# Optimization experiments

Measured on AMD Instinct MI355X. Metric: run time of the kernel, lower is better.

Reference implementation:

```python
import jax, jax.numpy as jnp
import numpy as np

N_GRAPHS = 262144
NPG = 6          # players per Rocket League graph
N_NODES = N_GRAPHS * NPG
HIDDEN = 32
FEAT = 4


def _build_edges():
    # fully-connected directed edges within each 6-node graph (30 per graph)
    s, d = np.meshgrid(np.arange(NPG), np.arange(NPG), indexing='ij')
    m = s != d
    ts, td = s[m], d[m]                      # [30]
    off = (np.arange(N_GRAPHS, dtype=np.int64) * NPG)[:, None]
    src = (ts[None, :] + off).reshape(-1)
    dst = (td[None, :] + off).reshape(-1)
    return np.stack([src, dst]).astype(np.int32)  # [2, E]


def setup_inputs() -> dict:
    key = jax.random.key(0)
    ks = jax.random.split(key, 10)
    edge_index = jnp.asarray(_build_edges())
    E = edge_index.shape[1]
    batch = jnp.asarray(np.repeat(np.arange(N_GRAPHS, dtype=np.int32), NPG))
    return {
        'x': jax.random.normal(ks[0], (N_NODES, FEAT), dtype=jnp.float32),
        'edge_index': edge_index,
        'edge_weight': jax.random.uniform(ks[1], (E,), dtype=jnp.float32),
        'batch': batch,
        'W1': jax.random.normal(ks[2], (FEAT, HIDDEN), dtype=jnp.float32) * 0.5,
        'b1': jax.random.normal(ks[3], (HIDDEN,), dtype=jnp.float32) * 0.1,
        'W2': jax.random.normal(ks[4], (HIDDEN, HIDDEN), dtype=jnp.float32) * 0.18,
        'b2': jax.random.normal(ks[5], (HIDDEN,), dtype=jnp.float32) * 0.1,
        'Wo': jax.random.normal(ks[6], (HIDDEN, 1), dtype=jnp.float32) * 0.18,
        'bo': jax.random.normal(ks[7], (1,), dtype=jnp.float32) * 0.1,
        'Wb': jax.random.normal(ks[8], (HIDDEN, 1), dtype=jnp.float32) * 0.18,
        'bb': jax.random.normal(ks[9], (1,), dtype=jnp.float32) * 0.1,
    }


def _gcn_conv(x, W, b, src, dst, w, n_nodes):
    # PyG GCNConv: symmetric normalization with self-loops already appended
    h = x @ W                                            # [N, out]
    deg = jax.ops.segment_sum(w, dst, num_segments=n_nodes)
    dinv = jnp.where(deg > 0, jax.lax.rsqrt(deg), 0.0)
    norm = dinv[src] * w * dinv[dst]                     # [E]
    agg = jax.ops.segment_sum(norm[:, None] * h[src], dst, num_segments=n_nodes)
    return agg + b


def reference(x, edge_index, edge_weight, batch, W1, b1, W2, b2, Wo, bo, Wb, bb):
    n = x.shape[0]
    loop = jnp.arange(n, dtype=edge_index.dtype)
    src = jnp.concatenate([edge_index[0], loop])
    dst = jnp.concatenate([edge_index[1], loop])
    w = jnp.concatenate([edge_weight, jnp.ones((n,), edge_weight.dtype)])

    h = jax.nn.relu(_gcn_conv(x, W1, b1, src, dst, w, n))
    h = jax.nn.relu(_gcn_conv(h, W2, b2, src, dst, w, n))

    # global mean pool by graph
    n_graphs = N_GRAPHS
    sums = jax.ops.segment_sum(h, batch, num_segments=n_graphs)
    cnt = jax.ops.segment_sum(jnp.ones((n,), h.dtype), batch, num_segments=n_graphs)
    pooled = sums / jnp.maximum(cnt, 1.0)[:, None]       # [G, 32]

    orange = jax.nn.sigmoid(pooled @ Wo + bo)            # [G, 1]
    blue = jax.nn.sigmoid(pooled @ Wb + bb)              # [G, 1]
    return orange, blue
```

## Files before the change

kernel.cpp:

```cpp
#include <hip/hip_runtime.h>
#include <hip/hip_bf16.h>

#define G_TOTAL 262144
#define ITERS   2
#define WAVES   4
#define NBLK    4096

typedef short s8v __attribute__((ext_vector_type(8)));
typedef float f4v __attribute__((ext_vector_type(4)));

#define MFMA16(a,b,c) __builtin_amdgcn_mfma_f32_16x16x32_bf16(a,b,c,0,0,0)

__device__ __forceinline__ unsigned short f2bf(float f){
    union { __hip_bfloat16 h; unsigned short u; } cv;
    cv.h = __float2bfloat16(f);
    return cv.u;
}
__device__ __forceinline__ unsigned int pk2(float a, float b){
    return (unsigned int)f2bf(a) | ((unsigned int)f2bf(b) << 16);
}

union FragU { s8v s; uint4 u; };

#define ARENA 9728

__global__ __launch_bounds__(256, 4)
void gcn_wave(const float* __restrict__ x,
              const float* __restrict__ ew,
              const float* __restrict__ W1,
              const float* __restrict__ b1,
              const float* __restrict__ W2,
              const float* __restrict__ b2,
              const float* __restrict__ Wo,
              const float* __restrict__ bo,
              const float* __restrict__ Wb,
              const float* __restrict__ bb,
              float* __restrict__ out)
{
    __shared__ __align__(16) unsigned char LDS[WAVES*ARENA];
    __shared__ float obuf[2][64];

    const int tid = threadIdx.x;
    const int w   = tid >> 6;
    const int l   = tid & 63;
    const int lr  = l & 15;
    const int lq  = l >> 4;

    unsigned char* AR = LDS + w*ARENA;
    unsigned short* h1RW  = (unsigned short*)AR;
    float*          rsumW = (float*)AR;
    unsigned short* actTW = (unsigned short*)(AR + 5120);

    const int gB = l >> 3, dB = l & 7;
    const bool bandOK = (dB < 6);
    const int dBc = bandOK ? dB : 0;
    int eoff0, eoff1, eoff2, eoff3, eoff4, eoff5;
    {
        int eo[6];
        #pragma unroll
        for (int s = 0; s < 6; ++s)
            eo[s] = (s == dBc) ? gB*30
                               : gB*30 + s*5 + (dBc - (dBc > s ? 1 : 0));
        eoff0=eo[0]; eoff1=eo[1]; eoff2=eo[2]; eoff3=eo[3]; eoff4=eo[4]; eoff5=eo[5];
    }
    const int bstore = (gB*6 + dBc)*40 + 32;
    const bool dnOK = (lq == 0) && ((lr & 7) < 6);
    int xoff[4];
    {
        const int dn  = lr & 7;
        const int dnc = (dn < 6) ? dn : 0;
        #pragma unroll
        for (int mt = 0; mt < 4; ++mt)
            xoff[mt] = (2*mt + (lr >> 3))*24 + dnc*4;
    }
    const bool aggB  = (lq == (lr >> 3)) && ((lr & 7) < 6);
    const int  boffL = (lq*6 + (lr & 7))*40 + 32;

    s8v w1f[2], w2f[2];
    #pragma unroll
    for (int nt = 0; nt < 2; ++nt) {
        #pragma unroll
        for (int e = 0; e < 8; ++e) {
            const int k = lq*8 + e, col = lr + 16*nt;
            w1f[nt][e] = (k < 4) ? (short)f2bf(W1[k*32 + col]) : (short)0;
            w2f[nt][e] = (short)f2bf(W2[k*32 + col]);
        }
    }
    f4v cb1[2], cb2[2];
    float wor[2][4], wbr[2][4];
    #pragma unroll
    for (int mt = 0; mt < 2; ++mt)
        #pragma unroll
        for (int j = 0; j < 4; ++j) {
            const int ch = 16*mt + lq*4 + j;
            cb1[mt][j] = b1[ch];  cb2[mt][j] = b2[ch];
            wor[mt][j] = Wo[ch];  wbr[mt][j] = Wb[ch];
        }
    const float boS = bo[0], bbS = bb[0];

    const long base = (long)blockIdx.x*(32*ITERS) + w*8;

    float evl[2][6];
    uint2 xB[2][4];

    {
        const long gb30 = base*30;
        evl[0][0] = ew[gb30 + eoff0];  evl[0][1] = ew[gb30 + eoff1];
        evl[0][2] = ew[gb30 + eoff2];  evl[0][3] = ew[gb30 + eoff3];
        evl[0][4] = ew[gb30 + eoff4];  evl[0][5] = ew[gb30 + eoff5];
        if (lq == 0) {
            const float* xp = x + base*24;
            #pragma unroll
            for (int mt = 0; mt < 4; ++mt) {
                const float4 xv = *(const float4*)(xp + xoff[mt]);
                xB[0][mt] = make_uint2(pk2(xv.x, xv.y), pk2(xv.z, xv.w));
            }
        }
    }

    #pragma unroll
    for (int it = 0; it < ITERS; ++it) {
        const int  cbuf = it & 1, nbuf = cbuf ^ 1;
        const long gbW  = base + it*32;

        if (it + 1 < ITERS) {
            const long gb30 = (gbW + 32)*30;
            evl[nbuf][0] = ew[gb30 + eoff0];  evl[nbuf][1] = ew[gb30 + eoff1];
            evl[nbuf][2] = ew[gb30 + eoff2];  evl[nbuf][3] = ew[gb30 + eoff3];
            evl[nbuf][4] = ew[gb30 + eoff4];  evl[nbuf][5] = ew[gb30 + eoff5];
            if (lq == 0) {
                const float* xp = x + (gbW + 32)*24;
                #pragma unroll
                for (int mt = 0; mt < 4; ++mt) {
                    const float4 xv = *(const float4*)(xp + xoff[mt]);
                    xB[nbuf][mt] = make_uint2(pk2(xv.x, xv.y), pk2(xv.z, xv.w));
                }
            }
        }

        #pragma unroll
        for (int mt = 0; mt < 4; ++mt) {
            s8v a = {0,0,0,0,0,0,0,0};
            if (dnOK) {
                FragU ua; ua.u = make_uint4(xB[cbuf][mt].x, xB[cbuf][mt].y, 0u, 0u);
                a = ua.s;
            }
            #pragma unroll
            for (int nt = 0; nt < 2; ++nt) {
                f4v z = {0.f,0.f,0.f,0.f};
                f4v t = MFMA16(a, w1f[nt], z);
                *(uint2*)(actTW + (16*nt + lr)*72 + 16*mt + 4*lq) =
                    make_uint2(pk2(t[0],t[1]), pk2(t[2],t[3]));
            }
        }

        {
            const float ws0 = (dB==0) ? 1.0f : evl[cbuf][0];
            const float ws1 = (dB==1) ? 1.0f : evl[cbuf][1];
            const float ws2 = (dB==2) ? 1.0f : evl[cbuf][2];
            const float ws3 = (dB==3) ? 1.0f : evl[cbuf][3];
            const float ws4 = (dB==4) ? 1.0f : evl[cbuf][4];
            const float ws5 = (dB==5) ? 1.0f : evl[cbuf][5];
            const float dd  = rsqrtf(ws0+ws1+ws2+ws3+ws4+ws5);
            const int sb = l & 56;
            const float dv0 = __shfl(dd, sb+0), dv1 = __shfl(dd, sb+1);
            const float dv2 = __shfl(dd, sb+2), dv3 = __shfl(dd, sb+3);
            const float dv4 = __shfl(dd, sb+4), dv5 = __shfl(dd, sb+5);
            if (bandOK) {
                const uint4 bw = make_uint4(pk2(dd*ws0*dv0, dd*ws1*dv1),
                                            pk2(dd*ws2*dv2, dd*ws3*dv3),
                                            pk2(dd*ws4*dv4, dd*ws5*dv5), 0u);
                *(uint4*)(h1RW + bstore) = bw;
            }
        }

        uint4 bfrv[4];
        #pragma unroll
        for (int nt = 0; nt < 4; ++nt) {
            bfrv[nt] = aggB ? *(const uint4*)(h1RW + nt*480 + boffL)
                            : make_uint4(0u,0u,0u,0u);
            FragU ub; ub.u = bfrv[nt];
            #pragma unroll
            for (int mtc = 0; mtc < 2; ++mtc) {
                s8v afr = {0,0,0,0,0,0,0,0};
                if (lq < 2) {
                    FragU ua;
                    ua.u = *(const uint4*)(actTW + (16*mtc + lr)*72 + 16*nt + 8*lq);
                    afr = ua.s;
                }
                f4v dD = MFMA16(afr, ub.s, cb1[mtc]);
                const float h0 = fmaxf(dD[0], 0.f);
                const float h1v= fmaxf(dD[1], 0.f);
                const float h2v= fmaxf(dD[2], 0.f);
                const float h3v= fmaxf(dD[3], 0.f);
                *(uint2*)(h1RW + (16*nt + lr)*40 + 16*mtc + 4*lq) =
                    make_uint2(pk2(h0,h1v), pk2(h2v,h3v));
            }
        }

        #pragma unroll
        for (int mt = 0; mt < 4; ++mt) {
            FragU ua; ua.u = *(const uint4*)(h1RW + (16*mt + lr)*40 + 8*lq);
            const s8v a = ua.s;
            #pragma unroll
            for (int nt = 0; nt < 2; ++nt) {
                f4v z = {0.f,0.f,0.f,0.f};
                f4v t = MFMA16(a, w2f[nt], z);
                *(uint2*)(actTW + (16*nt + lr)*72 + 16*mt + 4*lq) =
                    make_uint2(pk2(t[0],t[1]), pk2(t[2],t[3]));
            }
        }

        #pragma unroll
        for (int nt = 0; nt < 4; ++nt) {
            FragU ub; ub.u = bfrv[nt];
            float po = 0.f, pb = 0.f;
            #pragma unroll
            for (int mtc = 0; mtc < 2; ++mtc) {
                s8v afr = {0,0,0,0,0,0,0,0};
                if (lq < 2) {
                    FragU ua;
                    ua.u = *(const uint4*)(actTW + (16*mtc + lr)*72 + 16*nt + 8*lq);
                    afr = ua.s;
                }
                f4v dD = MFMA16(afr, ub.s, cb2[mtc]);
                #pragma unroll
                for (int j = 0; j < 4; ++j) {
                    const float h = fmaxf(dD[j], 0.f);
                    po += h * wor[mtc][j];
                    pb += h * wbr[mtc][j];
                }
            }
            po += __shfl_xor(po, 16);  po += __shfl_xor(po, 32);
            pb += __shfl_xor(pb, 16);  pb += __shfl_xor(pb, 32);
            if (lq == 0)      rsumW[16*nt + lr]      = po;
            else if (lq == 1) rsumW[64 + 16*nt + lr] = pb;
        }

        if (l < 16) {
            const int head = l >> 3, gl = l & 7;
            const float* rs = rsumW + head*64 + gl*8;
            const float4 a4 = *(const float4*)rs;
            const float2 a2 = *(const float2*)(rs + 4);
            const float s6 = a4.x+a4.y+a4.z+a4.w+a2.x+a2.y;
            const float zz = s6*(1.f/6.f) + (head ? bbS : boS);
            obuf[head][it*32 + w*8 + gl] = 1.f/(1.f + __expf(-zz));
        }
    }

    __syncthreads();
    if (tid < 128) {
        const int head = tid >> 6, idx = tid & 63;
        out[(long)head*G_TOTAL + (long)blockIdx.x*64 + idx] = obuf[head][idx];
    }
}

extern "C" void kernel_launch(void* const* d_in, const int* in_sizes, int n_in,
                              void* d_out, int out_size, void* d_ws, size_t ws_size,
                              hipStream_t stream)
{
    const float* x  = (const float*)d_in[0];
    const float* ew = (const float*)d_in[2];
    const float* W1 = (const float*)d_in[4];
    const float* b1 = (const float*)d_in[5];
    const float* W2 = (const float*)d_in[6];
    const float* b2 = (const float*)d_in[7];
    const float* Wo = (const float*)d_in[8];
    const float* bo = (const float*)d_in[9];
    const float* Wb = (const float*)d_in[10];
    const float* bb = (const float*)d_in[11];
    float* out = (float*)d_out;

    hipLaunchKernelGGL(gcn_wave, dim3(NBLK), dim3(256), 0, stream,
                       x, ew, W1, b1, W2, b2, Wo, bo, Wb, bb, out);
}
```

Measured before the change: 51.32 us.

## Pack six-node graphs densely into 48-row tiles instead of padded 8-row slots

Switches from padding each 6-node graph to 8 rows (64 rows per wave, 4 M-tiles) to a dense layout of 48 rows (3 M-tiles). The normalized adjacency band now lives in a separate zero-filled LDS region and is read through per-lane computed offsets. This removes a quarter of the MFMA and LDS work per wave and shrinks the per-wave LDS arena. In exchange the band fragment loads become unaligned scalar reads, and the bandB zeroing plus the more complex index math add overhead.

```diff
diff --git a/kernel.cpp b/kernel.cpp
--- a/kernel.cpp
+++ b/kernel.cpp
@@ -22,7 +22,7 @@
 
 union FragU { s8v s; uint4 u; };
 
-#define ARENA 9728
+#define ARENA 8960
 
 __global__ __launch_bounds__(256, 4)
 void gcn_wave(const float* __restrict__ x,
@@ -49,59 +49,63 @@
     unsigned char* AR = LDS + w*ARENA;
     unsigned short* h1RW  = (unsigned short*)AR;
     float*          rsumW = (float*)AR;
-    unsigned short* actTW = (unsigned short*)(AR + 5120);
-
-    const int gB = l >> 3, dB = l & 7;
-    const bool bandOK = (dB < 6);
-    const int dBc = bandOK ? dB : 0;
+    unsigned short* actTW = (unsigned short*)(AR + 3840);
+    unsigned int*   bandB = (unsigned int*)(AR + 7424);
+
+    #pragma unroll
+    for (int i = 0; i < 6; ++i) bandB[l + 64*i] = 0u;
+
+    const int gB = l / 6, dB = l - 6*gB;
+    const bool bOK = (l < 48);
+    const int gBc = bOK ? gB : 0;
+    const int dBc = bOK ? dB : 0;
     int eoff0, eoff1, eoff2, eoff3, eoff4, eoff5;
     {
         int eo[6];
         #pragma unroll
         for (int s = 0; s < 6; ++s)
-            eo[s] = (s == dBc) ? gB*30
-                               : gB*30 + s*5 + (dBc - (dBc > s ? 1 : 0));
+            eo[s] = (s == dBc) ? gBc*30
+                               : gBc*30 + s*5 + (dBc - (dBc > s ? 1 : 0));
         eoff0=eo[0]; eoff1=eo[1]; eoff2=eo[2]; eoff3=eo[3]; eoff4=eo[4]; eoff5=eo[5];
     }
-    const int bstore = (gB*6 + dBc)*40 + 32;
-    const bool dnOK = (lq == 0) && ((lr & 7) < 6);
-    int xoff[4];
-    {
-        const int dn  = lr & 7;
-        const int dnc = (dn < 6) ? dn : 0;
-        #pragma unroll
-        for (int mt = 0; mt < 4; ++mt)
-            xoff[mt] = (2*mt + (lr >> 3))*24 + dnc*4;
-    }
-    const bool aggB  = (lq == (lr >> 3)) && ((lr & 7) < 6);
-    const int  boffL = (lq*6 + (lr & 7))*40 + 32;
+    const int sbB   = 6*gBc;
+    const int bcell = bOK ? l : 0;
+    int bAddr[3];
+    #pragma unroll
+    for (int nt = 0; nt < 3; ++nt) {
+        const int r  = 16*nt + lr;
+        const int g  = r / 6;
+        int s0 = (8*nt + 8*lq - 6*g) >> 1;
+        if (s0 < -3 || s0 > 2) s0 = -4;
+        bAddr[nt] = 8*r + 4 + s0;
+    }
 
     s8v w1f[2], w2f[2];
     #pragma unroll
-    for (int nt = 0; nt < 2; ++nt) {
+    for (int cn = 0; cn < 2; ++cn) {
         #pragma unroll
         for (int e = 0; e < 8; ++e) {
-            const int k = lq*8 + e, col = lr + 16*nt;
-            w1f[nt][e] = (k < 4) ? (short)f2bf(W1[k*32 + col]) : (short)0;
-            w2f[nt][e] = (short)f2bf(W2[k*32 + col]);
+            const int k = lq*8 + e, col = lr + 16*cn;
+            w1f[cn][e] = (k < 4) ? (short)f2bf(W1[k*32 + col]) : (short)0;
+            w2f[cn][e] = (short)f2bf(W2[k*32 + col]);
         }
     }
     f4v cb1[2], cb2[2];
     float wor[2][4], wbr[2][4];
     #pragma unroll
-    for (int mt = 0; mt < 2; ++mt)
+    for (int mtc = 0; mtc < 2; ++mtc)
         #pragma unroll
         for (int j = 0; j < 4; ++j) {
-            const int ch = 16*mt + lq*4 + j;
-            cb1[mt][j] = b1[ch];  cb2[mt][j] = b2[ch];
-            wor[mt][j] = Wo[ch];  wbr[mt][j] = Wb[ch];
+            const int ch = 16*mtc + lq*4 + j;
+            cb1[mtc][j] = b1[ch];  cb2[mtc][j] = b2[ch];
+            wor[mtc][j] = Wo[ch];  wbr[mtc][j] = Wb[ch];
         }
     const float boS = bo[0], bbS = bb[0];
 
     const long base = (long)blockIdx.x*(32*ITERS) + w*8;
 
     float evl[2][6];
-    uint2 xB[2][4];
+    uint2 xB[2][3];
 
     {
         const long gb30 = base*30;
@@ -111,8 +115,8 @@
         if (lq == 0) {
             const float* xp = x + base*24;
             #pragma unroll
-            for (int mt = 0; mt < 4; ++mt) {
-                const float4 xv = *(const float4*)(xp + xoff[mt]);
+            for (int mt = 0; mt < 3; ++mt) {
+                const float4 xv = *(const float4*)(xp + (16*mt + lr)*4);
                 xB[0][mt] = make_uint2(pk2(xv.x, xv.y), pk2(xv.z, xv.w));
             }
         }
@@ -131,25 +135,25 @@
             if (lq == 0) {
                 const float* xp = x + (gbW + 32)*24;
                 #pragma unroll
-                for (int mt = 0; mt < 4; ++mt) {
-                    const float4 xv = *(const float4*)(xp + xoff[mt]);
+                for (int mt = 0; mt < 3; ++mt) {
+                    const float4 xv = *(const float4*)(xp + (16*mt + lr)*4);
                     xB[nbuf][mt] = make_uint2(pk2(xv.x, xv.y), pk2(xv.z, xv.w));
                 }
             }
         }
 
         #pragma unroll
-        for (int mt = 0; mt < 4; ++mt) {
+        for (int mt = 0; mt < 3; ++mt) {
             s8v a = {0,0,0,0,0,0,0,0};
-            if (dnOK) {
+            if (lq == 0) {
                 FragU ua; ua.u = make_uint4(xB[cbuf][mt].x, xB[cbuf][mt].y, 0u, 0u);
                 a = ua.s;
             }
             #pragma unroll
-            for (int nt = 0; nt < 2; ++nt) {
+            for (int cn = 0; cn < 2; ++cn) {
                 f4v z = {0.f,0.f,0.f,0.f};
-                f4v t = MFMA16(a, w1f[nt], z);
-                *(uint2*)(actTW + (16*nt + lr)*72 + 16*mt + 4*lq) =
+                f4v t = MFMA16(a, w1f[cn], z);
+                *(uint2*)(actTW + (16*cn + lr)*56 + 16*mt + 4*lq) =
                     make_uint2(pk2(t[0],t[1]), pk2(t[2],t[3]));
             }
         }
@@ -162,33 +166,30 @@
             const float ws4 = (dB==4) ? 1.0f : evl[cbuf][4];
             const float ws5 = (dB==5) ? 1.0f : evl[cbuf][5];
             const float dd  = rsqrtf(ws0+ws1+ws2+ws3+ws4+ws5);
-            const int sb = l & 56;
-            const float dv0 = __shfl(dd, sb+0), dv1 = __shfl(dd, sb+1);
-            const float dv2 = __shfl(dd, sb+2), dv3 = __shfl(dd, sb+3);
-            const float dv4 = __shfl(dd, sb+4), dv5 = __shfl(dd, sb+5);
-            if (bandOK) {
+            const float dv0 = __shfl(dd, sbB+0), dv1 = __shfl(dd, sbB+1);
+            const float dv2 = __shfl(dd, sbB+2), dv3 = __shfl(dd, sbB+3);
+            const float dv4 = __shfl(dd, sbB+4), dv5 = __shfl(dd, sbB+5);
+            if (bOK) {
                 const uint4 bw = make_uint4(pk2(dd*ws0*dv0, dd*ws1*dv1),
                                             pk2(dd*ws2*dv2, dd*ws3*dv3),
                                             pk2(dd*ws4*dv4, dd*ws5*dv5), 0u);
-                *(uint4*)(h1RW + bstore) = bw;
-            }
-        }
-
-        uint4 bfrv[4];
-        #pragma unroll
-        for (int nt = 0; nt < 4; ++nt) {
-            bfrv[nt] = aggB ? *(const uint4*)(h1RW + nt*480 + boffL)
-                            : make_uint4(0u,0u,0u,0u);
+                *(uint4*)(bandB + bcell*8 + 4) = bw;
+            }
+        }
+
+        uint4 bfrv[3];
+        #pragma unroll
+        for (int nt = 0; nt < 3; ++nt) {
+            {
+                const unsigned int* bp = bandB + bAddr[nt];
+                bfrv[nt] = make_uint4(bp[0], bp[1], bp[2], bp[3]);
+            }
             FragU ub; ub.u = bfrv[nt];
             #pragma unroll
             for (int mtc = 0; mtc < 2; ++mtc) {
-                s8v afr = {0,0,0,0,0,0,0,0};
-                if (lq < 2) {
-                    FragU ua;
-                    ua.u = *(const uint4*)(actTW + (16*mtc + lr)*72 + 16*nt + 8*lq);
-                    afr = ua.s;
-                }
-                f4v dD = MFMA16(afr, ub.s, cb1[mtc]);
+                FragU ua;
+                ua.u = *(const uint4*)(actTW + (16*mtc + lr)*56 + 8*nt + 8*lq);
+                f4v dD = MFMA16(ua.s, ub.s, cb1[mtc]);
                 const float h0 = fmaxf(dD[0], 0.f);
                 const float h1v= fmaxf(dD[1], 0.f);
                 const float h2v= fmaxf(dD[2], 0.f);
@@ -199,31 +200,27 @@
         }
 
         #pragma unroll
-        for (int mt = 0; mt < 4; ++mt) {
+        for (int mt = 0; mt < 3; ++mt) {
             FragU ua; ua.u = *(const uint4*)(h1RW + (16*mt + lr)*40 + 8*lq);
             const s8v a = ua.s;
             #pragma unroll
-            for (int nt = 0; nt < 2; ++nt) {
+            for (int cn = 0; cn < 2; ++cn) {
                 f4v z = {0.f,0.f,0.f,0.f};
-                f4v t = MFMA16(a, w2f[nt], z);
-                *(uint2*)(actTW + (16*nt + lr)*72 + 16*mt + 4*lq) =
+                f4v t = MFMA16(a, w2f[cn], z);
+                *(uint2*)(actTW + (16*cn + lr)*56 + 16*mt + 4*lq) =
                     make_uint2(pk2(t[0],t[1]), pk2(t[2],t[3]));
             }
         }
 
         #pragma unroll
-        for (int nt = 0; nt < 4; ++nt) {
+        for (int nt = 0; nt < 3; ++nt) {
             FragU ub; ub.u = bfrv[nt];
             float po = 0.f, pb = 0.f;
             #pragma unroll
             for (int mtc = 0; mtc < 2; ++mtc) {
-                s8v afr = {0,0,0,0,0,0,0,0};
-                if (lq < 2) {
-                    FragU ua;
-                    ua.u = *(const uint4*)(actTW + (16*mtc + lr)*72 + 16*nt + 8*lq);
-                    afr = ua.s;
-                }
-                f4v dD = MFMA16(afr, ub.s, cb2[mtc]);
+                FragU ua;
+                ua.u = *(const uint4*)(actTW + (16*mtc + lr)*56 + 8*nt + 8*lq);
+                f4v dD = MFMA16(ua.s, ub.s, cb2[mtc]);
                 #pragma unroll
                 for (int j = 0; j < 4; ++j) {
                     const float h = fmaxf(dD[j], 0.f);
@@ -234,15 +231,16 @@
             po += __shfl_xor(po, 16);  po += __shfl_xor(po, 32);
             pb += __shfl_xor(pb, 16);  pb += __shfl_xor(pb, 32);
             if (lq == 0)      rsumW[16*nt + lr]      = po;
-            else if (lq == 1) rsumW[64 + 16*nt + lr] = pb;
+            else if (lq == 1) rsumW[48 + 16*nt + lr] = pb;
         }
 
         if (l < 16) {
             const int head = l >> 3, gl = l & 7;
-            const float* rs = rsumW + head*64 + gl*8;
-            const float4 a4 = *(const float4*)rs;
+            const float* rs = rsumW + head*48 + gl*6;
+            const float2 a0 = *(const float2*)rs;
+            const float2 a1 = *(const float2*)(rs + 2);
             const float2 a2 = *(const float2*)(rs + 4);
-            const float s6 = a4.x+a4.y+a4.z+a4.w+a2.x+a2.y;
+            const float s6 = a0.x+a0.y+a1.x+a1.y+a2.x+a2.y;
             const float zz = s6*(1.f/6.f) + (head ? bbS : boS);
             obuf[head][it*32 + w*8 + gl] = 1.f/(1.f + __expf(-zz));
         }
```

New measurement: 45.11 us. 1.14x faster.
